# Optimization experiments

Hardware: AMD Instinct MI355X
Metric: run time of the kernel (lower is better)

The kernel has to match this reference:

```python
import jax, jax.numpy as jnp
import numpy as np

B, L, D_MODEL, D_FF, H = 2, 2048, 512, 512, 8
DK = D_FF // H


def _lin(key, fan_in, fan_out):
    k1, k2 = jax.random.split(key)
    lim = 1.0 / np.sqrt(fan_in)
    W = jax.random.uniform(k1, (fan_in, fan_out), jnp.float32, -lim, lim)
    b = jax.random.uniform(k2, (fan_out,), jnp.float32, -lim, lim)
    return W, b


def setup_inputs() -> dict:
    key = jax.random.key(0)
    ks = jax.random.split(key, 13)
    x = jax.random.normal(ks[0], (B, L, D_MODEL), jnp.float32)
    x_knowledge = jax.random.normal(ks[1], (B, L, D_MODEL), jnp.float32)
    Wv, bv = _lin(ks[2], D_MODEL, D_FF)
    Wk, bk = _lin(ks[3], D_MODEL, D_FF)
    Wq, bq = _lin(ks[4], D_MODEL, D_FF)
    Wkf, bkf = _lin(ks[5], D_MODEL, D_FF)
    Wqf, bqf = _lin(ks[6], D_MODEL, D_FF)
    Wq2, bq2 = _lin(ks[7], D_FF, D_FF)
    Wk2, bk2 = _lin(ks[8], D_FF, D_FF)
    Wkf2, bkf2 = _lin(ks[9], D_FF, D_FF)
    Wqf2, bqf2 = _lin(ks[10], D_FF, D_FF)
    Wo, bo = _lin(ks[11], D_FF, D_MODEL)
    return dict(x=x, x_knowledge=x_knowledge, Wv=Wv, bv=bv, Wk=Wk, bk=bk,
                Wq=Wq, bq=bq, Wkf=Wkf, bkf=bkf, Wqf=Wqf, bqf=bqf,
                Wq2=Wq2, bq2=bq2, Wk2=Wk2, bk2=bk2, Wqf2=Wqf2, bqf2=bqf2,
                Wkf2=Wkf2, bkf2=bkf2, Wo=Wo, bo=bo)


def reference(x, x_knowledge, Wv, bv, Wk, bk, Wq, bq, Wkf, bkf, Wqf, bqf,
              Wq2, bq2, Wk2, bk2, Wqf2, bqf2, Wkf2, bkf2, Wo, bo):
    b, l, _ = x.shape
    # first projections from d_model -> d_ff
    v = x @ Wv + bv
    k = x @ Wk + bk
    q = x @ Wq + bq
    k_fei = x_knowledge @ Wkf + bkf
    q_fei = x_knowledge @ Wqf + bqf
    # second projections + NONSTANDARD head split: raw reshape (B,L,d_ff)->(B,h,L,dk)
    q = (q @ Wq2 + bq2).reshape(b, H, l, DK)
    k = (k @ Wk2 + bk2).reshape(b, H, l, DK)
    q_fei = (q_fei @ Wqf2 + bqf2).reshape(b, H, l, DK)
    k_fei = (k_fei @ Wkf2 + bkf2).reshape(b, H, l, DK)
    scale = 1.0 / np.sqrt(2.0 * DK).astype(np.float32)
    att = jnp.einsum('bhld,bhmd->bhlm', q, k) * scale
    att_fei = jnp.einsum('bhld,bhmd->bhlm', q_fei, k_fei) * scale
    score = jax.nn.softmax(att + att_fei, axis=-1)  # dropout is identity at eval
    v = v.reshape(b, H, l, DK)
    out = jnp.einsum('bhlm,bhmd->bhld', score, v).reshape(b, l, D_FF)
    return out @ Wo + bo
```

## Files before the change

kernel.cpp:

```cpp
#include <hip/hip_runtime.h>
#include <hip/hip_bf16.h>

typedef unsigned short u16;
typedef unsigned int   u32;
typedef __attribute__((ext_vector_type(8))) short bf16x8;
typedef __attribute__((ext_vector_type(4))) float f32x4;

#define SCALE 0.08838834764831845f
#define SCLOG 0.12752040542575836f

__device__ inline u16 f2bf(float f) {
  u32 u = __builtin_bit_cast(u32, f);
  u = (u + 0x7FFFu + ((u >> 16) & 1u)) >> 16;
  return (u16)u;
}
__device__ inline float bf2f(u16 b) {
  u32 u = (u32)b << 16;
  return __builtin_bit_cast(float, u);
}
__device__ __forceinline__ u16 cvbf(float f) {
  return __builtin_bit_cast(u16, __float2bfloat16(f));
}
__device__ __forceinline__ u32 pkbf(float a, float b) {
  return (u32)cvbf(a) | ((u32)cvbf(b) << 16);
}
__device__ __forceinline__ float fexp2(float x) {
#if __has_builtin(__builtin_amdgcn_exp2f)
  return __builtin_amdgcn_exp2f(x);
#else
  float r; asm("v_exp_f32 %0, %1" : "=v"(r) : "v"(x)); return r;
#endif
}

__device__ __forceinline__ void glds16(const u16* g, u16* l) {
  __builtin_amdgcn_global_load_lds(
      (__attribute__((address_space(1))) void*)g,
      (__attribute__((address_space(3))) void*)l, 16, 0, 0);
}

struct CvPtrs { const float* in[6]; u16* out[6]; int nblk[6]; };

__global__ __launch_bounds__(256) void cvtAll(CvPtrs cp) {
  const int y = blockIdx.y;
  if ((int)blockIdx.x >= cp.nblk[y]) return;
  const float* in = cp.in[y];
  u16* out = cp.out[y];
  const int i = (blockIdx.x * 256 + threadIdx.x) * 8;
  float4 f0 = *(const float4*)(in + i);
  float4 f1 = *(const float4*)(in + i + 4);
  alignas(16) u16 t[8] = {f2bf(f0.x), f2bf(f0.y), f2bf(f0.z), f2bf(f0.w),
                          f2bf(f1.x), f2bf(f1.y), f2bf(f1.z), f2bf(f1.w)};
  *(uint4*)(out + i) = *(const uint4*)t;
}

struct WPtrs { const float* w[10]; const float* b[10]; };
__constant__ const int ZMAP[6] = {0, 5, 6, 7, 8, 9};

__global__ __launch_bounds__(256) void transposeW(WPtrs p, u16* __restrict__ out,
                                                  float* __restrict__ biasP) {
  __shared__ u16 ts[64][65];
  const int z = ZMAP[blockIdx.z];
  const float sc = (z == 5 || z == 7) ? SCLOG : 1.0f;
  const float* in = p.w[z];
  u16* o = out + (size_t)z * 262144;
  const int t = threadIdx.x;
  const int k0 = blockIdx.y * 64, n0 = blockIdx.x * 64;
  if (blockIdx.x == 0 && blockIdx.y == 0 && (z == 0 || z == 9)) {
    biasP[z * 512 + t]       = p.b[z][t];
    biasP[z * 512 + t + 256] = p.b[z][t + 256];
  }
  for (int pp = 0; pp < 16; ++pp) {
    int id = t + 256 * pp; int r = id >> 6, c = id & 63;
    ts[r][c] = f2bf(in[(size_t)(k0 + r) * 512 + n0 + c] * sc);
  }
  __syncthreads();
  for (int pp = 0; pp < 16; ++pp) {
    int id = t + 256 * pp; int r = id >> 6, c = id & 63;
    o[(size_t)(n0 + r) * 512 + k0 + c] = ts[c][r];
  }
}

struct BEPtrs { const float* b1[4]; const float* w2[4]; const float* b2[4]; };

__global__ __launch_bounds__(256) void biasEff(BEPtrs be, float* __restrict__ biasP) {
  __shared__ float red[16][17];
  const int z = blockIdx.x;
  const int n0 = blockIdx.y * 16;
  const float sc = (z == 0 || z == 2) ? SCLOG : 1.0f;
  const int nl = threadIdx.x & 15, jg = threadIdx.x >> 4;
  const float* b1 = be.b1[z];
  const float* w2 = be.w2[z];
  float s = 0.0f;
  #pragma unroll 4
  for (int jj = 0; jj < 32; ++jj) {
    const int j = jg * 32 + jj;
    s += b1[j] * w2[(size_t)j * 512 + n0 + nl];
  }
  red[jg][nl] = s;
  __syncthreads();
  if (threadIdx.x < 16) {
    float t = 0.0f;
    #pragma unroll
    for (int g = 0; g < 16; ++g) t += red[g][threadIdx.x];
    biasP[(1 + z) * 512 + n0 + threadIdx.x] =
        (t + be.b2[z][n0 + threadIdx.x]) * sc;
  }
}

struct GemmBatch {
  const u16* A[4];
  const u16* Ax;
  int xsplit;
  void* out[5];
  int wrow0, zstride;
};

template <typename TOUT, bool NB>
__device__ __forceinline__ void gemm_body(const GemmBatch& gb,
    const u16* __restrict__ Wt, const float* __restrict__ biasP,
    int tx, int my, int z) {
  const u16* A = (tx < gb.xsplit) ? gb.A[z] : gb.Ax;
  const int wrow = gb.wrow0 + z * gb.zstride + tx * 128;
  const int m0 = my * 128;
  const u16* B = Wt + (size_t)wrow * 512;
  const float* bias = biasP + wrow;

  const int t = threadIdx.x, wid = t >> 6, lane = t & 63;
  const int lg = lane >> 4, ln = lane & 15;
  const int wr = wid >> 1, wc = wid & 1;

  __shared__ u16 As[128][64];
  __shared__ u16 Bs[128][64];

  const u16* Ag = A + (size_t)m0 * 512;
  const int lrow = lane >> 3, lch = lane & 7;

  f32x4 acc[4][4];
  #pragma unroll
  for (int i = 0; i < 4; ++i)
    #pragma unroll
    for (int j = 0; j < 4; ++j)
      #pragma unroll
      for (int r = 0; r < 4; ++r) acc[i][j][r] = 0.0f;

  for (int kt = 0; kt < 8; ++kt) {
    #pragma unroll
    for (int c = 0; c < 4; ++c) {
      const int row = (wid * 4 + c) * 8 + lrow;
      const size_t go = (size_t)row * 512 + kt * 64 + lch * 8;
      glds16(Ag + go, &As[(wid * 4 + c) * 8][0]);
      glds16(B  + go, &Bs[(wid * 4 + c) * 8][0]);
    }
    __syncthreads();

    #pragma unroll
    for (int ck = 0; ck < 2; ++ck) {
      bf16x8 af[4], bfr[4];
      #pragma unroll
      for (int mi = 0; mi < 4; ++mi)
        af[mi] = *(const bf16x8*)&As[wr * 64 + mi * 16 + ln][ck * 32 + lg * 8];
      #pragma unroll
      for (int ni = 0; ni < 4; ++ni)
        bfr[ni] = *(const bf16x8*)&Bs[wc * 64 + ni * 16 + ln][ck * 32 + lg * 8];
      #pragma unroll
      for (int mi = 0; mi < 4; ++mi)
        #pragma unroll
        for (int ni = 0; ni < 4; ++ni)
          acc[mi][ni] = __builtin_amdgcn_mfma_f32_16x16x32_bf16(
              af[mi], bfr[ni], acc[mi][ni], 0, 0, 0);
    }
    if (kt < 7) __syncthreads();
  }

  TOUT* C = (TOUT*)gb.out[(wrow >> 9) - (gb.wrow0 >> 9)];
  const int nbase = wrow & 511;
  #pragma unroll
  for (int ni = 0; ni < 4; ++ni) {
    const int colw = wc * 64 + ni * 16 + ln;
    const float bv = NB ? 0.0f : bias[colw];
    const int col = nbase + colw;
    #pragma unroll
    for (int mi = 0; mi < 4; ++mi)
      #pragma unroll
      for (int r = 0; r < 4; ++r) {
        const int row = m0 + wr * 64 + mi * 16 + 4 * lg + r;
        const float val = acc[mi][ni][r] + bv;
        if constexpr (sizeof(TOUT) == 4) C[(size_t)row * 512 + col] = val;
        else                             C[(size_t)row * 512 + col] = cvbf(val);
      }
  }
}

template <typename TOUT, bool NB>
__global__ __launch_bounds__(256, 4) void gemm4(GemmBatch gb,
    const u16* __restrict__ Wt, const float* __restrict__ biasP) {
  gemm_body<TOUT, NB>(gb, Wt, biasP, blockIdx.x, blockIdx.y, blockIdx.z);
}

__global__ __launch_bounds__(256, 4) void gemm5(GemmBatch gb,
    const u16* __restrict__ Wt, const float* __restrict__ biasP) {
  const int id = blockIdx.x;
  const int nid = (id & 7) * 80 + (id >> 3);
  const int tx = nid % 20, my = nid / 20;
  gemm_body<u16, false>(gb, Wt, biasP, tx, my, 0);
}

__global__ __launch_bounds__(256) void transposeV(const u16* __restrict__ v1,
                                                  u16* __restrict__ vt) {
  __shared__ u16 ts[64][65];
  const size_t base = (size_t)blockIdx.y * 131072;
  const u16* in = v1 + base;
  u16* out = vt + base;
  const int l0 = blockIdx.x * 64;
  const int t = threadIdx.x;
  const int r = t >> 3, c8 = (t & 7) * 8;
  for (int pp = 0; pp < 2; ++pp) {
    int rr = r + pp * 32;
    *(uint4*)&ts[rr][c8] = *(const uint4*)&in[(size_t)(l0 + rr) * 64 + c8];
  }
  __syncthreads();
  for (int pp = 0; pp < 2; ++pp) {
    int d = r + pp * 32;
    alignas(16) u16 tmp[8];
    #pragma unroll
    for (int i = 0; i < 8; ++i) tmp[i] = ts[c8 + i][d];
    *(uint4*)&out[(size_t)d * 2048 + l0 + c8] = *(const uint4*)tmp;
  }
}

__global__ __launch_bounds__(512) void attn9(
    const u16* __restrict__ q2, const u16* __restrict__ k2,
    const u16* __restrict__ qf2, const u16* __restrict__ kf2,
    const u16* __restrict__ vtg, u16* __restrict__ opart,
    float2* __restrict__ mlbuf) {
  const int id = blockIdx.x;
  const int nid = (id & 7) * 32 + (id >> 3);
  const int split = nid & 1;
  const int qt = (nid >> 1) & 7;
  const int bh = nid >> 4;
  const size_t base = (size_t)bh * 131072;
  const int kv0 = split * 1024;

  const u16* Q  = q2  + base;
  const u16* Qf = qf2 + base;
  u16* Op = opart + (size_t)split * 2097152 + base;

  const int t = threadIdx.x, wid = t >> 6, lane = t & 63;
  const int lg = lane >> 4, ln = lane & 15;
  const int r0 = qt * 256 + wid * 32;

  __shared__ u16 K_s [2][64][64];
  __shared__ u16 Kf_s[2][64][64];
  __shared__ u16 Vt_s[2][64][64];

  const int srow = t >> 3, sch = t & 7;
  const int fsr = (srow & 3) | (((srow >> 3) & 1) << 2);
  const int sw = (sch ^ fsr) * 8;
  const u16* Ksrc  = k2  + base + (size_t)(kv0 + srow) * 64 + sch * 8;
  const u16* Kfsrc = kf2 + base + (size_t)(kv0 + srow) * 64 + sch * 8;
  const u16* Vsrc  = vtg + base + (size_t)srow * 2048 + kv0 + sch * 8;

  bf16x8 aq[2][4];
  #pragma unroll
  for (int qb = 0; qb < 2; ++qb) {
    const int row = r0 + qb * 16 + ln;
    aq[qb][0] = *(const bf16x8*)&Q [row * 64 +      lg * 8];
    aq[qb][1] = *(const bf16x8*)&Q [row * 64 + 32 + lg * 8];
    aq[qb][2] = *(const bf16x8*)&Qf[row * 64 +      lg * 8];
    aq[qb][3] = *(const bf16x8*)&Qf[row * 64 + 32 + lg * 8];
  }

  f32x4 oacc[2][4];
  #pragma unroll
  for (int qb = 0; qb < 2; ++qb)
    #pragma unroll
    for (int df = 0; df < 4; ++df)
      #pragma unroll
      for (int r = 0; r < 4; ++r) oacc[qb][df][r] = 0.0f;
  float m_run[2], l_par[2];
  #pragma unroll
  for (int qb = 0; qb < 2; ++qb) { m_run[qb] = -1e30f; l_par[qb] = 0.0f; }

  const int rbase = 8 * (ln >> 2) + (ln & 3);

  uint4 rk = *(const uint4*)(Ksrc);
  uint4 rf = *(const uint4*)(Kfsrc);
  uint4 rv = *(const uint4*)(Vsrc);
  *(uint4*)&K_s [0][srow][sw] = rk;
  *(uint4*)&Kf_s[0][srow][sw] = rf;
  *(uint4*)&Vt_s[0][srow][sw] = rv;
  __syncthreads();

  int cur = 0;
  for (int kt = 0; kt < 16; ++kt) {
    if (kt < 15) {
      const int ko = (kt + 1) * 4096;
      rk = *(const uint4*)(Ksrc  + ko);
      rf = *(const uint4*)(Kfsrc + ko);
      rv = *(const uint4*)(Vsrc  + (kt + 1) * 64);
    }

    f32x4 s[2][4];
    __builtin_amdgcn_s_setprio(1);
    #pragma unroll
    for (int m = 0; m < 4; ++m) {
      const int rowg = rbase + 4 * (m & 1) + 32 * (m >> 1);
      const int fz = (rowg & 3) | (((rowg >> 3) & 1) << 2);
      bf16x8 a0 = *(const bf16x8*)&K_s [cur][rowg][((0 + lg) ^ fz) * 8];
      bf16x8 a1 = *(const bf16x8*)&K_s [cur][rowg][((4 + lg) ^ fz) * 8];
      bf16x8 a2 = *(const bf16x8*)&Kf_s[cur][rowg][((0 + lg) ^ fz) * 8];
      bf16x8 a3 = *(const bf16x8*)&Kf_s[cur][rowg][((4 + lg) ^ fz) * 8];
      #pragma unroll
      for (int qb = 0; qb < 2; ++qb) {
        f32x4 a;
        #pragma unroll
        for (int r = 0; r < 4; ++r) a[r] = 0.0f;
        a = __builtin_amdgcn_mfma_f32_16x16x32_bf16(a0, aq[qb][0], a, 0, 0, 0);
        a = __builtin_amdgcn_mfma_f32_16x16x32_bf16(a1, aq[qb][1], a, 0, 0, 0);
        a = __builtin_amdgcn_mfma_f32_16x16x32_bf16(a2, aq[qb][2], a, 0, 0, 0);
        a = __builtin_amdgcn_mfma_f32_16x16x32_bf16(a3, aq[qb][3], a, 0, 0, 0);
        s[qb][m] = a;
      }
    }
    __builtin_amdgcn_s_setprio(0);

    float smax[2];
    bool viol = false;
    #pragma unroll
    for (int qb = 0; qb < 2; ++qb) {
      float vm[4];
      #pragma unroll
      for (int m = 0; m < 4; ++m)
        vm[m] = fmaxf(fmaxf(s[qb][m][0], s[qb][m][1]),
                      fmaxf(s[qb][m][2], s[qb][m][3]));
      smax[qb] = fmaxf(fmaxf(vm[0], vm[1]), fmaxf(vm[2], vm[3]));
      viol = viol || (smax[qb] > m_run[qb] + 11.0f);
    }
    if (__any(viol)) {
      float corrq[2];
      #pragma unroll
      for (int qb = 0; qb < 2; ++qb) {
        float v = smax[qb];
        v = fmaxf(v, __shfl_xor(v, 16, 64));
        v = fmaxf(v, __shfl_xor(v, 32, 64));
        const float mnew = fmaxf(m_run[qb], v);
        corrq[qb] = fexp2(m_run[qb] - mnew);
        m_run[qb] = mnew;
        l_par[qb] *= corrq[qb];
      }
      #pragma unroll
      for (int qb = 0; qb < 2; ++qb)
        #pragma unroll
        for (int r = 0; r < 4; ++r) {
          const float c = __shfl(corrq[qb], 4 * lg + r, 64);
          #pragma unroll
          for (int df = 0; df < 4; ++df) oacc[qb][df][r] *= c;
        }
    }

    bf16x8 pa[2][2];
    #pragma unroll
    for (int qb = 0; qb < 2; ++qb) {
      float pf[4][4], ps[4];
      #pragma unroll
      for (int m = 0; m < 4; ++m) {
        #pragma unroll
        for (int r = 0; r < 4; ++r)
          pf[m][r] = fexp2(s[qb][m][r] - m_run[qb]);
        ps[m] = (pf[m][0] + pf[m][1]) + (pf[m][2] + pf[m][3]);
      }
      l_par[qb] += (ps[0] + ps[1]) + (ps[2] + ps[3]);
      #pragma unroll
      for (int kc = 0; kc < 2; ++kc) {
        union { u32 w[4]; bf16x8 v; } U;
        U.w[0] = pkbf(pf[2 * kc][0],     pf[2 * kc][1]);
        U.w[1] = pkbf(pf[2 * kc][2],     pf[2 * kc][3]);
        U.w[2] = pkbf(pf[2 * kc + 1][0], pf[2 * kc + 1][1]);
        U.w[3] = pkbf(pf[2 * kc + 1][2], pf[2 * kc + 1][3]);
        pa[qb][kc] = U.v;
      }
    }

    __builtin_amdgcn_s_setprio(1);
    #pragma unroll
    for (int kc = 0; kc < 2; ++kc)
      #pragma unroll
      for (int df = 0; df < 4; ++df) {
        const int rv = 16 * df + ln;
        const int fz = (rv & 3) | (((rv >> 3) & 1) << 2);
        bf16x8 bv = *(const bf16x8*)&Vt_s[cur][rv][((kc * 4 + lg) ^ fz) * 8];
        oacc[0][df] = __builtin_amdgcn_mfma_f32_16x16x32_bf16(pa[0][kc], bv, oacc[0][df], 0, 0, 0);
        oacc[1][df] = __builtin_amdgcn_mfma_f32_16x16x32_bf16(pa[1][kc], bv, oacc[1][df], 0, 0, 0);
      }
    __builtin_amdgcn_s_setprio(0);

    if (kt < 15) {
      *(uint4*)&K_s [cur ^ 1][srow][sw] = rk;
      *(uint4*)&Kf_s[cur ^ 1][srow][sw] = rf;
      *(uint4*)&Vt_s[cur ^ 1][srow][sw] = rv;
      __syncthreads();
      cur ^= 1;
    }
  }

  #pragma unroll
  for (int qb = 0; qb < 2; ++qb) {
    l_par[qb] += __shfl_xor(l_par[qb], 16, 64);
    l_par[qb] += __shfl_xor(l_par[qb], 32, 64);
  }

  #pragma unroll
  for (int qb = 0; qb < 2; ++qb)
    #pragma unroll
    for (int df = 0; df < 4; ++df)
      #pragma unroll
      for (int r = 0; r < 4; ++r) {
        const int row = r0 + qb * 16 + 4 * lg + r;
        const int col = df * 16 + ln;
        Op[(size_t)row * 64 + col] = cvbf(oacc[qb][df][r]);
      }
  if (lane < 16) {
    #pragma unroll
    for (int qb = 0; qb < 2; ++qb) {
      const int grow = bh * 2048 + r0 + qb * 16 + ln;
      mlbuf[split * 32768 + grow] = make_float2(m_run[qb], l_par[qb]);
    }
  }
}

__global__ __launch_bounds__(256) void combine(
    const u16* __restrict__ opart, const float2* __restrict__ mlbuf,
    u16* __restrict__ att) {
  const int gid = blockIdx.x * 256 + threadIdx.x;
  const int row = gid >> 3, c8 = (gid & 7) * 8;
  const float2 ml1 = mlbuf[row];
  const float2 ml2 = mlbuf[32768 + row];
  const float mx = fmaxf(ml1.x, ml2.x);
  const float a1 = fexp2(ml1.x - mx), a2 = fexp2(ml2.x - mx);
  const float inv = 1.0f / (ml1.y * a1 + ml2.y * a2);
  const float w1 = a1 * inv, w2 = a2 * inv;
  uint4 o1 = *(const uint4*)&opart[(size_t)row * 64 + c8];
  uint4 o2 = *(const uint4*)&opart[2097152 + (size_t)row * 64 + c8];
  const u16* p1 = (const u16*)&o1;
  const u16* p2 = (const u16*)&o2;
  alignas(16) u16 ot[8];
  #pragma unroll
  for (int i = 0; i < 8; ++i)
    ot[i] = cvbf(bf2f(p1[i]) * w1 + bf2f(p2[i]) * w2);
  *(uint4*)&att[(size_t)row * 64 + c8] = *(const uint4*)ot;
}

extern "C" void kernel_launch(void* const* d_in, const int* in_sizes, int n_in,
                              void* d_out, int out_size, void* d_ws, size_t ws_size,
                              hipStream_t stream) {
  const float* x    = (const float*)d_in[0];
  const float* xk   = (const float*)d_in[1];
  const float* Wv   = (const float*)d_in[2];  const float* bv   = (const float*)d_in[3];
  const float* Wk   = (const float*)d_in[4];  const float* bk   = (const float*)d_in[5];
  const float* Wq   = (const float*)d_in[6];  const float* bq   = (const float*)d_in[7];
  const float* Wkf  = (const float*)d_in[8];  const float* bkf  = (const float*)d_in[9];
  const float* Wqf  = (const float*)d_in[10]; const float* bqf  = (const float*)d_in[11];
  const float* Wq2  = (const float*)d_in[12]; const float* bq2  = (const float*)d_in[13];
  const float* Wk2  = (const float*)d_in[14]; const float* bk2  = (const float*)d_in[15];
  const float* Wqf2 = (const float*)d_in[16]; const float* bqf2 = (const float*)d_in[17];
  const float* Wkf2 = (const float*)d_in[18]; const float* bkf2 = (const float*)d_in[19];
  const float* Wo   = (const float*)d_in[20]; const float* bo   = (const float*)d_in[21];

  u16* ws = (u16*)d_ws;
  u16* Wt = ws;
  float* biasP = (float*)(ws + 2621440);
  u16* bufs = ws + 2621440 + 10240;
  const size_t BUF = 2097152;
  u16* b0 = bufs + 0 * BUF;
  u16* b1 = bufs + 1 * BUF;
  u16* b2 = bufs + 2 * BUF;
  u16* b3 = bufs + 3 * BUF;
  u16* b5 = bufs + 5 * BUF;
  u16* b6 = bufs + 6 * BUF;
  u16* b7 = bufs + 7 * BUF;
  u16* b8 = bufs + 8 * BUF;
  float2* mlbuf = (float2*)(bufs + 9 * BUF);
  u16* W1b = bufs + 9 * BUF + 262144;

  CvPtrs cp;
  cp.in[0] = x;   cp.out[0] = b5;             cp.nblk[0] = 1024;
  cp.in[1] = xk;  cp.out[1] = b6;             cp.nblk[1] = 1024;
  cp.in[2] = Wq;  cp.out[2] = W1b;            cp.nblk[2] = 128;
  cp.in[3] = Wk;  cp.out[3] = W1b + 262144;   cp.nblk[3] = 128;
  cp.in[4] = Wqf; cp.out[4] = W1b + 524288;   cp.nblk[4] = 128;
  cp.in[5] = Wkf; cp.out[5] = W1b + 786432;   cp.nblk[5] = 128;
  cvtAll<<<dim3(1024, 6), 256, 0, stream>>>(cp);

  WPtrs wp;
  wp.w[0] = Wv;  wp.w[1] = Wk;  wp.w[2] = Wq;   wp.w[3] = Wkf;  wp.w[4] = Wqf;
  wp.w[5] = Wq2; wp.w[6] = Wk2; wp.w[7] = Wqf2; wp.w[8] = Wkf2; wp.w[9] = Wo;
  wp.b[0] = bv;  wp.b[1] = bk;  wp.b[2] = bq;   wp.b[3] = bkf;  wp.b[4] = bqf;
  wp.b[5] = bq2; wp.b[6] = bk2; wp.b[7] = bqf2; wp.b[8] = bkf2; wp.b[9] = bo;
  transposeW<<<dim3(8, 8, 6), 256, 0, stream>>>(wp, Wt, biasP);

  GemmBatch gw = {};
  gw.A[0] = Wt + 5 * 262144; gw.A[1] = Wt + 6 * 262144;
  gw.A[2] = Wt + 7 * 262144; gw.A[3] = Wt + 8 * 262144;
  gw.Ax = gw.A[0]; gw.xsplit = 100;
  gw.out[0] = Wt + 1 * 262144; gw.out[1] = Wt + 2 * 262144;
  gw.out[2] = Wt + 3 * 262144; gw.out[3] = Wt + 4 * 262144;
  gw.wrow0 = 0; gw.zstride = 512;
  gemm4<u16, true><<<dim3(4, 4, 4), 256, 0, stream>>>(gw, W1b, biasP);

  BEPtrs be;
  be.b1[0] = bq;  be.w2[0] = Wq2;  be.b2[0] = bq2;
  be.b1[1] = bk;  be.w2[1] = Wk2;  be.b2[1] = bk2;
  be.b1[2] = bqf; be.w2[2] = Wqf2; be.b2[2] = bqf2;
  be.b1[3] = bkf; be.w2[3] = Wkf2; be.b2[3] = bkf2;
  biasEff<<<dim3(4, 32), 256, 0, stream>>>(be, biasP);

  GemmBatch g1 = {};
  g1.A[0] = b5;  g1.Ax = b6;  g1.xsplit = 12;
  g1.out[0] = b0; g1.out[1] = b1; g1.out[2] = b3; g1.out[3] = b7; g1.out[4] = b8;
  g1.wrow0 = 0; g1.zstride = 0;
  gemm5<<<dim3(640), 256, 0, stream>>>(g1, Wt, biasP);

  transposeV<<<dim3(32, 16), 256, 0, stream>>>(b0, b2);

  attn9<<<dim3(256), 512, 0, stream>>>(b1, b3, b7, b8, b2, b5, mlbuf);

  combine<<<dim3(1024), 256, 0, stream>>>(b5, mlbuf, b0);

  GemmBatch g4 = {};
  g4.A[0] = b0; g4.Ax = b0; g4.xsplit = 100;
  g4.out[0] = d_out;
  g4.wrow0 = 4608; g4.zstride = 0;
  gemm4<float, false><<<dim3(4, 32, 1), 256, 0, stream>>>(g4, Wt, biasP);
}
```

Baseline: 106.0 us.

## Merge prep kernels and rework attention to 4-way KV split with 1024-thread blocks

Folds the conversion, weight-transpose and bias-folding kernels into one prep launch, cutting two kernel launches. The attention kernel moves from a 2-way to a 4-way KV split with 512 query rows per block and 16 waves. K/Kf staging is divided between the two halves of the block, and the s_setprio hints are removed. The combine step now merges four partial outputs, which adds partial-output traffic and a larger workspace region.

```diff
diff --git a/kernel.cpp b/kernel.cpp
--- a/kernel.cpp
+++ b/kernel.cpp
@@ -38,72 +38,73 @@
       (__attribute__((address_space(3))) void*)l, 16, 0, 0);
 }
 
-struct CvPtrs { const float* in[6]; u16* out[6]; int nblk[6]; };
-
-__global__ __launch_bounds__(256) void cvtAll(CvPtrs cp) {
-  const int y = blockIdx.y;
-  if ((int)blockIdx.x >= cp.nblk[y]) return;
-  const float* in = cp.in[y];
-  u16* out = cp.out[y];
-  const int i = (blockIdx.x * 256 + threadIdx.x) * 8;
-  float4 f0 = *(const float4*)(in + i);
-  float4 f1 = *(const float4*)(in + i + 4);
-  alignas(16) u16 t[8] = {f2bf(f0.x), f2bf(f0.y), f2bf(f0.z), f2bf(f0.w),
-                          f2bf(f1.x), f2bf(f1.y), f2bf(f1.z), f2bf(f1.w)};
-  *(uint4*)(out + i) = *(const uint4*)t;
-}
-
-struct WPtrs { const float* w[10]; const float* b[10]; };
+struct PrepArgs {
+  const float* cin[6]; u16* cout[6]; int cnblk[6];
+  const float* w[10];  const float* b[10]; u16* Wt; float* biasP;
+  const float* b1[4]; const float* w2[4]; const float* b2[4];
+};
 __constant__ const int ZMAP[6] = {0, 5, 6, 7, 8, 9};
 
-__global__ __launch_bounds__(256) void transposeW(WPtrs p, u16* __restrict__ out,
-                                                  float* __restrict__ biasP) {
+__global__ __launch_bounds__(256) void prep(PrepArgs p) {
   __shared__ u16 ts[64][65];
-  const int z = ZMAP[blockIdx.z];
-  const float sc = (z == 5 || z == 7) ? SCLOG : 1.0f;
-  const float* in = p.w[z];
-  u16* o = out + (size_t)z * 262144;
-  const int t = threadIdx.x;
-  const int k0 = blockIdx.y * 64, n0 = blockIdx.x * 64;
-  if (blockIdx.x == 0 && blockIdx.y == 0 && (z == 0 || z == 9)) {
-    biasP[z * 512 + t]       = p.b[z][t];
-    biasP[z * 512 + t + 256] = p.b[z][t + 256];
-  }
-  for (int pp = 0; pp < 16; ++pp) {
-    int id = t + 256 * pp; int r = id >> 6, c = id & 63;
-    ts[r][c] = f2bf(in[(size_t)(k0 + r) * 512 + n0 + c] * sc);
-  }
-  __syncthreads();
-  for (int pp = 0; pp < 16; ++pp) {
-    int id = t + 256 * pp; int r = id >> 6, c = id & 63;
-    o[(size_t)(n0 + r) * 512 + k0 + c] = ts[c][r];
-  }
-}
-
-struct BEPtrs { const float* b1[4]; const float* w2[4]; const float* b2[4]; };
-
-__global__ __launch_bounds__(256) void biasEff(BEPtrs be, float* __restrict__ biasP) {
   __shared__ float red[16][17];
-  const int z = blockIdx.x;
-  const int n0 = blockIdx.y * 16;
-  const float sc = (z == 0 || z == 2) ? SCLOG : 1.0f;
-  const int nl = threadIdx.x & 15, jg = threadIdx.x >> 4;
-  const float* b1 = be.b1[z];
-  const float* w2 = be.w2[z];
-  float s = 0.0f;
-  #pragma unroll 4
-  for (int jj = 0; jj < 32; ++jj) {
-    const int j = jg * 32 + jj;
-    s += b1[j] * w2[(size_t)j * 512 + n0 + nl];
-  }
-  red[jg][nl] = s;
-  __syncthreads();
-  if (threadIdx.x < 16) {
-    float t = 0.0f;
-    #pragma unroll
-    for (int g = 0; g < 16; ++g) t += red[g][threadIdx.x];
-    biasP[(1 + z) * 512 + n0 + threadIdx.x] =
-        (t + be.b2[z][n0 + threadIdx.x]) * sc;
+  const int y = blockIdx.y, bx = blockIdx.x, t = threadIdx.x;
+
+  if (y < 6) {
+    if (bx >= p.cnblk[y]) return;
+    const float* in = p.cin[y];
+    u16* out = p.cout[y];
+    const int i = (bx * 256 + t) * 8;
+    float4 f0 = *(const float4*)(in + i);
+    float4 f1 = *(const float4*)(in + i + 4);
+    alignas(16) u16 tt[8] = {f2bf(f0.x), f2bf(f0.y), f2bf(f0.z), f2bf(f0.w),
+                             f2bf(f1.x), f2bf(f1.y), f2bf(f1.z), f2bf(f1.w)};
+    *(uint4*)(out + i) = *(const uint4*)tt;
+    return;
+  }
+  if (bx < 384) {
+    const int z = ZMAP[bx >> 6];
+    const int tile = bx & 63;
+    const int n0 = (tile & 7) * 64, k0 = (tile >> 3) * 64;
+    const float sc = (z == 5 || z == 7) ? SCLOG : 1.0f;
+    const float* in = p.w[z];
+    u16* o = p.Wt + (size_t)z * 262144;
+    if (tile == 0 && (z == 0 || z == 9)) {
+      p.biasP[z * 512 + t]       = p.b[z][t];
+      p.biasP[z * 512 + t + 256] = p.b[z][t + 256];
+    }
+    for (int pp = 0; pp < 16; ++pp) {
+      int id = t + 256 * pp; int r = id >> 6, c = id & 63;
+      ts[r][c] = f2bf(in[(size_t)(k0 + r) * 512 + n0 + c] * sc);
+    }
+    __syncthreads();
+    for (int pp = 0; pp < 16; ++pp) {
+      int id = t + 256 * pp; int r = id >> 6, c = id & 63;
+      o[(size_t)(n0 + r) * 512 + k0 + c] = ts[c][r];
+    }
+    return;
+  }
+  if (bx < 512) {
+    const int v = bx - 384;
+    const int z = v >> 5, n0 = (v & 31) * 16;
+    const float sc = (z == 0 || z == 2) ? SCLOG : 1.0f;
+    const int nl = t & 15, jg = t >> 4;
+    const float* b1 = p.b1[z];
+    const float* w2 = p.w2[z];
+    float s = 0.0f;
+    #pragma unroll 4
+    for (int jj = 0; jj < 32; ++jj) {
+      const int j = jg * 32 + jj;
+      s += b1[j] * w2[(size_t)j * 512 + n0 + nl];
+    }
+    red[jg][nl] = s;
+    __syncthreads();
+    if (t < 16) {
+      float tt = 0.0f;
+      #pragma unroll
+      for (int g = 0; g < 16; ++g) tt += red[g][t];
+      p.biasP[(1 + z) * 512 + n0 + t] = (tt + p.b2[z][n0 + t]) * sc;
+    }
   }
 }
 
@@ -228,18 +229,18 @@
   }
 }
 
-__global__ __launch_bounds__(512) void attn9(
+__global__ __launch_bounds__(1024) void attn10(
     const u16* __restrict__ q2, const u16* __restrict__ k2,
     const u16* __restrict__ qf2, const u16* __restrict__ kf2,
     const u16* __restrict__ vtg, u16* __restrict__ opart,
     float2* __restrict__ mlbuf) {
   const int id = blockIdx.x;
   const int nid = (id & 7) * 32 + (id >> 3);
-  const int split = nid & 1;
-  const int qt = (nid >> 1) & 7;
+  const int split = nid & 3;
+  const int qt = (nid >> 2) & 3;
   const int bh = nid >> 4;
   const size_t base = (size_t)bh * 131072;
-  const int kv0 = split * 1024;
+  const int kv0 = split * 512;
 
   const u16* Q  = q2  + base;
   const u16* Qf = qf2 + base;
@@ -247,18 +248,19 @@
 
   const int t = threadIdx.x, wid = t >> 6, lane = t & 63;
   const int lg = lane >> 4, ln = lane & 15;
-  const int r0 = qt * 256 + wid * 32;
+  const int r0 = qt * 512 + wid * 32;
 
   __shared__ u16 K_s [2][64][64];
   __shared__ u16 Kf_s[2][64][64];
   __shared__ u16 Vt_s[2][64][64];
 
-  const int srow = t >> 3, sch = t & 7;
+  const int th = t & 511;
+  const int srow = th >> 3, sch = th & 7;
   const int fsr = (srow & 3) | (((srow >> 3) & 1) << 2);
   const int sw = (sch ^ fsr) * 8;
-  const u16* Ksrc  = k2  + base + (size_t)(kv0 + srow) * 64 + sch * 8;
-  const u16* Kfsrc = kf2 + base + (size_t)(kv0 + srow) * 64 + sch * 8;
-  const u16* Vsrc  = vtg + base + (size_t)srow * 2048 + kv0 + sch * 8;
+  const bool lo = (t < 512);
+  const u16* src0 = (lo ? k2 : kf2) + base + (size_t)(kv0 + srow) * 64 + sch * 8;
+  const u16* srcV = vtg + base + (size_t)srow * 2048 + kv0 + sch * 8;
 
   bf16x8 aq[2][4];
   #pragma unroll
@@ -283,25 +285,25 @@
 
   const int rbase = 8 * (ln >> 2) + (ln & 3);
 
-  uint4 rk = *(const uint4*)(Ksrc);
-  uint4 rf = *(const uint4*)(Kfsrc);
-  uint4 rv = *(const uint4*)(Vsrc);
-  *(uint4*)&K_s [0][srow][sw] = rk;
-  *(uint4*)&Kf_s[0][srow][sw] = rf;
-  *(uint4*)&Vt_s[0][srow][sw] = rv;
+  uint4 rk = *(const uint4*)(src0);
+  uint4 rv;
+  if (lo) rv = *(const uint4*)(srcV);
+  if (lo) {
+    *(uint4*)&K_s [0][srow][sw] = rk;
+    *(uint4*)&Vt_s[0][srow][sw] = rv;
+  } else {
+    *(uint4*)&Kf_s[0][srow][sw] = rk;
+  }
   __syncthreads();
 
   int cur = 0;
-  for (int kt = 0; kt < 16; ++kt) {
-    if (kt < 15) {
-      const int ko = (kt + 1) * 4096;
-      rk = *(const uint4*)(Ksrc  + ko);
-      rf = *(const uint4*)(Kfsrc + ko);
-      rv = *(const uint4*)(Vsrc  + (kt + 1) * 64);
+  for (int kt = 0; kt < 8; ++kt) {
+    if (kt < 7) {
+      rk = *(const uint4*)(src0 + (kt + 1) * 4096);
+      if (lo) rv = *(const uint4*)(srcV + (kt + 1) * 64);
     }
 
     f32x4 s[2][4];
-    __builtin_amdgcn_s_setprio(1);
     #pragma unroll
     for (int m = 0; m < 4; ++m) {
       const int rowg = rbase + 4 * (m & 1) + 32 * (m >> 1);
@@ -322,7 +324,6 @@
         s[qb][m] = a;
       }
     }
-    __builtin_amdgcn_s_setprio(0);
 
     float smax[2];
     bool viol = false;
@@ -381,23 +382,24 @@
       }
     }
 
-    __builtin_amdgcn_s_setprio(1);
     #pragma unroll
     for (int kc = 0; kc < 2; ++kc)
       #pragma unroll
       for (int df = 0; df < 4; ++df) {
-        const int rv = 16 * df + ln;
-        const int fz = (rv & 3) | (((rv >> 3) & 1) << 2);
-        bf16x8 bv = *(const bf16x8*)&Vt_s[cur][rv][((kc * 4 + lg) ^ fz) * 8];
+        const int rv_ = 16 * df + ln;
+        const int fz = (rv_ & 3) | (((rv_ >> 3) & 1) << 2);
+        bf16x8 bv = *(const bf16x8*)&Vt_s[cur][rv_][((kc * 4 + lg) ^ fz) * 8];
         oacc[0][df] = __builtin_amdgcn_mfma_f32_16x16x32_bf16(pa[0][kc], bv, oacc[0][df], 0, 0, 0);
         oacc[1][df] = __builtin_amdgcn_mfma_f32_16x16x32_bf16(pa[1][kc], bv, oacc[1][df], 0, 0, 0);
       }
-    __builtin_amdgcn_s_setprio(0);
-
-    if (kt < 15) {
-      *(uint4*)&K_s [cur ^ 1][srow][sw] = rk;
-      *(uint4*)&Kf_s[cur ^ 1][srow][sw] = rf;
-      *(uint4*)&Vt_s[cur ^ 1][srow][sw] = rv;
+
+    if (kt < 7) {
+      if (lo) {
+        *(uint4*)&K_s [cur ^ 1][srow][sw] = rk;
+        *(uint4*)&Vt_s[cur ^ 1][srow][sw] = rv;
+      } else {
+        *(uint4*)&Kf_s[cur ^ 1][srow][sw] = rk;
+      }
       __syncthreads();
       cur ^= 1;
     }
@@ -428,26 +430,35 @@
   }
 }
 
-__global__ __launch_bounds__(256) void combine(
-    const u16* __restrict__ opart, const float2* __restrict__ mlbuf,
+__global__ __launch_bounds__(256) void combine4(
+    const u16* __restrict__ op, const float2* __restrict__ ml,
     u16* __restrict__ att) {
   const int gid = blockIdx.x * 256 + threadIdx.x;
   const int row = gid >> 3, c8 = (gid & 7) * 8;
-  const float2 ml1 = mlbuf[row];
-  const float2 ml2 = mlbuf[32768 + row];
-  const float mx = fmaxf(ml1.x, ml2.x);
-  const float a1 = fexp2(ml1.x - mx), a2 = fexp2(ml2.x - mx);
-  const float inv = 1.0f / (ml1.y * a1 + ml2.y * a2);
-  const float w1 = a1 * inv, w2 = a2 * inv;
-  uint4 o1 = *(const uint4*)&opart[(size_t)row * 64 + c8];
-  uint4 o2 = *(const uint4*)&opart[2097152 + (size_t)row * 64 + c8];
-  const u16* p1 = (const u16*)&o1;
-  const u16* p2 = (const u16*)&o2;
+  const float2 m0 = ml[row];
+  const float2 m1 = ml[32768 + row];
+  const float2 m2 = ml[65536 + row];
+  const float2 m3 = ml[98304 + row];
+  const float mx = fmaxf(fmaxf(m0.x, m1.x), fmaxf(m2.x, m3.x));
+  const float a0 = fexp2(m0.x - mx), a1 = fexp2(m1.x - mx);
+  const float a2 = fexp2(m2.x - mx), a3 = fexp2(m3.x - mx);
+  const float inv = 1.0f / (m0.y * a0 + m1.y * a1 + m2.y * a2 + m3.y * a3);
+  const float w0 = a0 * inv, w1 = a1 * inv, w2 = a2 * inv, w3 = a3 * inv;
+  const size_t o = (size_t)row * 64 + c8;
+  uint4 v0 = *(const uint4*)&op[o];
+  uint4 v1 = *(const uint4*)&op[2097152 + o];
+  uint4 v2 = *(const uint4*)&op[4194304 + o];
+  uint4 v3 = *(const uint4*)&op[6291456 + o];
+  const u16* p0 = (const u16*)&v0;
+  const u16* p1 = (const u16*)&v1;
+  const u16* p2 = (const u16*)&v2;
+  const u16* p3 = (const u16*)&v3;
   alignas(16) u16 ot[8];
   #pragma unroll
   for (int i = 0; i < 8; ++i)
-    ot[i] = cvbf(bf2f(p1[i]) * w1 + bf2f(p2[i]) * w2);
-  *(uint4*)&att[(size_t)row * 64 + c8] = *(const uint4*)ot;
+    ot[i] = cvbf(bf2f(p0[i]) * w0 + bf2f(p1[i]) * w1 +
+                 bf2f(p2[i]) * w2 + bf2f(p3[i]) * w3);
+  *(uint4*)&att[o] = *(const uint4*)ot;
 }
 
 extern "C" void kernel_launch(void* const* d_in, const int* in_sizes, int n_in,
@@ -480,23 +491,26 @@
   u16* b7 = bufs + 7 * BUF;
   u16* b8 = bufs + 8 * BUF;
   float2* mlbuf = (float2*)(bufs + 9 * BUF);
-  u16* W1b = bufs + 9 * BUF + 262144;
-
-  CvPtrs cp;
-  cp.in[0] = x;   cp.out[0] = b5;             cp.nblk[0] = 1024;
-  cp.in[1] = xk;  cp.out[1] = b6;             cp.nblk[1] = 1024;
-  cp.in[2] = Wq;  cp.out[2] = W1b;            cp.nblk[2] = 128;
-  cp.in[3] = Wk;  cp.out[3] = W1b + 262144;   cp.nblk[3] = 128;
-  cp.in[4] = Wqf; cp.out[4] = W1b + 524288;   cp.nblk[4] = 128;
-  cp.in[5] = Wkf; cp.out[5] = W1b + 786432;   cp.nblk[5] = 128;
-  cvtAll<<<dim3(1024, 6), 256, 0, stream>>>(cp);
-
-  WPtrs wp;
-  wp.w[0] = Wv;  wp.w[1] = Wk;  wp.w[2] = Wq;   wp.w[3] = Wkf;  wp.w[4] = Wqf;
-  wp.w[5] = Wq2; wp.w[6] = Wk2; wp.w[7] = Wqf2; wp.w[8] = Wkf2; wp.w[9] = Wo;
-  wp.b[0] = bv;  wp.b[1] = bk;  wp.b[2] = bq;   wp.b[3] = bkf;  wp.b[4] = bqf;
-  wp.b[5] = bq2; wp.b[6] = bk2; wp.b[7] = bqf2; wp.b[8] = bkf2; wp.b[9] = bo;
-  transposeW<<<dim3(8, 8, 6), 256, 0, stream>>>(wp, Wt, biasP);
+  u16* W1b = bufs + 9 * BUF + 524288;
+  u16* opart = W1b + 1048576;
+
+  PrepArgs pa = {};
+  pa.cin[0] = x;   pa.cout[0] = b5;             pa.cnblk[0] = 1024;
+  pa.cin[1] = xk;  pa.cout[1] = b6;             pa.cnblk[1] = 1024;
+  pa.cin[2] = Wq;  pa.cout[2] = W1b;            pa.cnblk[2] = 128;
+  pa.cin[3] = Wk;  pa.cout[3] = W1b + 262144;   pa.cnblk[3] = 128;
+  pa.cin[4] = Wqf; pa.cout[4] = W1b + 524288;   pa.cnblk[4] = 128;
+  pa.cin[5] = Wkf; pa.cout[5] = W1b + 786432;   pa.cnblk[5] = 128;
+  pa.w[0] = Wv;  pa.w[1] = Wk;  pa.w[2] = Wq;   pa.w[3] = Wkf;  pa.w[4] = Wqf;
+  pa.w[5] = Wq2; pa.w[6] = Wk2; pa.w[7] = Wqf2; pa.w[8] = Wkf2; pa.w[9] = Wo;
+  pa.b[0] = bv;  pa.b[1] = bk;  pa.b[2] = bq;   pa.b[3] = bkf;  pa.b[4] = bqf;
+  pa.b[5] = bq2; pa.b[6] = bk2; pa.b[7] = bqf2; pa.b[8] = bkf2; pa.b[9] = bo;
+  pa.Wt = Wt; pa.biasP = biasP;
+  pa.b1[0] = bq;  pa.w2[0] = Wq2;  pa.b2[0] = bq2;
+  pa.b1[1] = bk;  pa.w2[1] = Wk2;  pa.b2[1] = bk2;
+  pa.b1[2] = bqf; pa.w2[2] = Wqf2; pa.b2[2] = bqf2;
+  pa.b1[3] = bkf; pa.w2[3] = Wkf2; pa.b2[3] = bkf2;
+  prep<<<dim3(1024, 7), 256, 0, stream>>>(pa);
 
   GemmBatch gw = {};
   gw.A[0] = Wt + 5 * 262144; gw.A[1] = Wt + 6 * 262144;
@@ -507,13 +521,6 @@
   gw.wrow0 = 0; gw.zstride = 512;
   gemm4<u16, true><<<dim3(4, 4, 4), 256, 0, stream>>>(gw, W1b, biasP);
 
-  BEPtrs be;
-  be.b1[0] = bq;  be.w2[0] = Wq2;  be.b2[0] = bq2;
-  be.b1[1] = bk;  be.w2[1] = Wk2;  be.b2[1] = bk2;
-  be.b1[2] = bqf; be.w2[2] = Wqf2; be.b2[2] = bqf2;
-  be.b1[3] = bkf; be.w2[3] = Wkf2; be.b2[3] = bkf2;
-  biasEff<<<dim3(4, 32), 256, 0, stream>>>(be, biasP);
-
   GemmBatch g1 = {};
   g1.A[0] = b5;  g1.Ax = b6;  g1.xsplit = 12;
   g1.out[0] = b0; g1.out[1] = b1; g1.out[2] = b3; g1.out[3] = b7; g1.out[4] = b8;
@@ -522,9 +529,9 @@
 
   transposeV<<<dim3(32, 16), 256, 0, stream>>>(b0, b2);
 
-  attn9<<<dim3(256), 512, 0, stream>>>(b1, b3, b7, b8, b2, b5, mlbuf);
-
-  combine<<<dim3(1024), 256, 0, stream>>>(b5, mlbuf, b0);
+  attn10<<<dim3(256), 1024, 0, stream>>>(b1, b3, b7, b8, b2, opart, mlbuf);
+
+  combine4<<<dim3(1024), 256, 0, stream>>>(opart, mlbuf, b0);
 
   GemmBatch g4 = {};
   g4.A[0] = b0; g4.Ax = b0; g4.xsplit = 100;
```

New measurement: 116.3 us. 9.7% more time.
